# Kernel tuning notes

Hardware: AMD Instinct MI355X
Metric: run time of the kernel (lower is better)

## Reference

```python
import jax, jax.numpy as jnp
from jax import lax
import numpy as np

NUM_LABELS = 15
LABEL_TO_ID = {"O": 0, "B-PERSON": 1, "I-PERSON": 2, "B-LOCATION": 3, "I-LOCATION": 4,
               "B-ORGANIZATION": 5, "I-ORGANIZATION": 6, "B-PHONE": 7, "I-PHONE": 8,
               "B-EMAIL": 9, "I-EMAIL": 10, "B-ID_NUMBER": 11, "I-ID_NUMBER": 12,
               "B-ADDRESS": 13, "I-ADDRESS": 14}


def _pii_constraints():
    """Replicates EnhancedPIICRF._setup_transition_constraints."""
    forbidden = -10000.0
    c = np.zeros((NUM_LABELS, NUM_LABELS), dtype=np.float32)
    pii_types = ['PERSON', 'LOCATION', 'ORGANIZATION', 'PHONE', 'EMAIL', 'ID_NUMBER', 'ADDRESS']
    for t in pii_types:
        b_idx = LABEL_TO_ID[f'B-{t}']
        i_idx = LABEL_TO_ID[f'I-{t}']
        for o in pii_types:
            if o != t:
                c[LABEL_TO_ID[f'B-{o}'], i_idx] = forbidden
        if t in ['PHONE', 'EMAIL', 'ID_NUMBER']:
            c[i_idx, i_idx] = -1.0
    return jnp.asarray(c)


def setup_inputs() -> dict:
    key = jax.random.key(0)
    k1, k2, k3, k4, k5 = jax.random.split(key, 5)
    B, T, L = 512, 4096, NUM_LABELS
    emissions = jax.random.normal(k1, (B, T, L), dtype=jnp.float32)
    labels = jax.random.randint(k2, (B, T), 0, L, dtype=jnp.int64)
    mask = jnp.ones((B, T), dtype=jnp.bool_)
    # torchcrf init: uniform(-0.1, 0.1); constraints added to transitions
    transitions = jax.random.uniform(k3, (L, L), jnp.float32, -0.1, 0.1) + _pii_constraints()
    start_transitions = jax.random.uniform(k4, (L,), jnp.float32, -0.1, 0.1)
    end_transitions = jax.random.uniform(k5, (L,), jnp.float32, -0.1, 0.1)
    return {"emissions": emissions, "transitions": transitions,
            "start_transitions": start_transitions, "end_transitions": end_transitions,
            "labels": labels, "mask": mask}


def reference(emissions, transitions, start_transitions, end_transitions, labels, mask):
    """loss = -mean log-likelihood (torchcrf reduction='mean')."""
    B, T, L = emissions.shape
    maskf = mask.astype(emissions.dtype)
    labels = labels.astype(jnp.int32)

    # ---- numerator: score of the gold path (fully vectorized) ----
    em_score = jnp.take_along_axis(emissions, labels[..., None], axis=2)[..., 0]  # [B,T]
    em_score = (em_score * maskf).sum(axis=1)
    trans_score = (transitions[labels[:, :-1], labels[:, 1:]] * maskf[:, 1:]).sum(axis=1)
    seq_ends = mask.sum(axis=1).astype(jnp.int32) - 1
    last_tags = labels[jnp.arange(B), seq_ends]
    numerator = (start_transitions[labels[:, 0]] + em_score + trans_score
                 + end_transitions[last_tags])

    # ---- denominator: forward algorithm (log-sum-exp recurrence) ----
    alpha0 = start_transitions[None, :] + emissions[:, 0]  # [B,L]

    def step(alpha, xs):
        em_t, m_t = xs  # [B,L], [B]
        nxt = jax.nn.logsumexp(alpha[:, :, None] + transitions[None], axis=1) + em_t
        return jnp.where(m_t[:, None], nxt, alpha), None

    em_T = jnp.swapaxes(emissions, 0, 1)[1:]   # [T-1,B,L]
    mk_T = jnp.swapaxes(mask, 0, 1)[1:]        # [T-1,B]
    alpha, _ = lax.scan(step, alpha0, (em_T, mk_T))
    denominator = jax.nn.logsumexp(alpha + end_transitions[None, :], axis=1)

    llh = numerator - denominator
    return -jnp.mean(llh)
```

## Files before the change

### kernel.cpp

```cpp
#include <hip/hip_runtime.h>


typedef __attribute__((ext_vector_type(8))) __bf16 bf16x8;
typedef __attribute__((ext_vector_type(4))) float f32x4;
typedef __attribute__((ext_vector_type(2))) float f32x2;

#define BATCH 512
#define TLEN  4096
#define NCH   16
#define CLEN  256
#define LOG2E 1.44269504088896340736f
#define LN2   0.69314718055994530942f

__device__ __forceinline__ int pack_bf16_pair(float lo, float hi){
  return __builtin_amdgcn_perm(__float_as_uint(hi), __float_as_uint(lo), 0x07060302);
}

__global__ __launch_bounds__(256) void crf_chunk_kernel(
    const float* __restrict__ em, const float* __restrict__ trans,
    const int* __restrict__ labels,
    float* __restrict__ wsM, float* __restrict__ wsS, float* __restrict__ wsNum)
{
  const int tid   = threadIdx.x;
  const int lane  = tid & 63;
  const int col   = lane & 15;
  const int g     = lane >> 4;
  const int wid   = blockIdx.x * 4 + (tid >> 6);
  const int b     = wid >> 4;
  const int c     = wid & (NCH - 1);
  const int t0    = 1 + c * CLEN;
  const int steps = (c == NCH - 1) ? (CLEN - 1) : CLEN;
  const int colc  = (col < 15) ? col : 14;
  const long bT   = (long)b * TLEN;

  {
    const int tA = c * CLEN + lane * 4;
    const int4 lv = *reinterpret_cast<const int4*>(labels + bT + tA);
    const int lpm1 = __shfl(lv.w, lane - 1);
    const float* emA = em + (bT + tA) * 15;
    float a = 0.f;
    float a0 = emA[lv.x] + trans[lpm1 * 15 + lv.x];
    if (lane > 0) a += a0;
    a += emA[15 + lv.y] + trans[lv.x * 15 + lv.y];
    a += emA[30 + lv.z] + trans[lv.y * 15 + lv.z];
    a += emA[45 + lv.w] + trans[lv.z * 15 + lv.w];
    if (lane == 63 && c < NCH - 1){
      const int te = (c + 1) * CLEN;
      const int le = labels[bT + te];
      a += em[(bT + te) * 15 + le] + trans[lv.w * 15 + le];
    }
    #pragma unroll
    for (int off = 1; off < 64; off <<= 1) a += __shfl_xor(a, off);
    if (lane == 0) wsNum[wid] = a;
  }

  f32x2 wa01, wa23;
  {
    float wv[4];
    #pragma unroll
    for (int j = 0; j < 4; ++j){
      const int row = 4 * g + j;
      wv[j] = (row < 15 && col < 15)
            ? __builtin_amdgcn_exp2f(trans[row * 15 + col] * LOG2E) : 0.f;
    }
    wa01.x = wv[0]; wa01.y = wv[1]; wa23.x = wv[2]; wa23.y = wv[3];
  }

  union { bf16x8 v; int i[4]; } af, bfr;
  af.i[2] = 0; af.i[3] = 0;
  bfr.i[2] = 0; bfr.i[3] = 0;

  f32x4 d;
  #pragma unroll
  for (int r = 0; r < 4; ++r) d[r] = (4 * g + r == col) ? 1.f : 0.f;

  const f32x4 zero4 = {0.f, 0.f, 0.f, 0.f};
  const float* emb = em + (bT + t0) * 15 + colc;
  float S = 0.f;
  const int rounds = steps >> 3;
  const int rem    = steps & 7;
  float eb[8];

  for (int r = 0; r < rounds; ++r){
    const float* p = emb + r * 120;
    #pragma unroll
    for (int u = 0; u < 8; ++u) eb[u] = p[u * 15];
    if (r){
      float m = fmaxf(fmaxf(d[0], d[1]), fmaxf(d[2], d[3]));
      m = fmaxf(m, __shfl_xor(m, 16));
      m = fmaxf(m, __shfl_xor(m, 32));
      m = fmaxf(m, 1e-30f);
      const float sc = __builtin_amdgcn_rcpf(m);
      S += __builtin_amdgcn_logf(m);
      d[0] *= sc; d[1] *= sc; d[2] *= sc; d[3] *= sc;
    }
    #pragma unroll
    for (int u = 0; u < 8; ++u){
      const float E = __builtin_amdgcn_exp2f(eb[u] * LOG2E);
      const f32x2 e01 = wa01 * E, e23 = wa23 * E;
      af.i[0]  = pack_bf16_pair(e01.x, e01.y);
      af.i[1]  = pack_bf16_pair(e23.x, e23.y);
      bfr.i[0] = pack_bf16_pair(d[0], d[1]);
      bfr.i[1] = pack_bf16_pair(d[2], d[3]);
      d = __builtin_amdgcn_mfma_f32_16x16x32_bf16(af.v, bfr.v, zero4, 0, 0, 0);
    }
  }

  if (rem){
    const float* p = emb + rounds * 120;
    float et[7];
    #pragma unroll
    for (int u = 0; u < 7; ++u) et[u] = p[u * 15];
    float m = fmaxf(fmaxf(d[0], d[1]), fmaxf(d[2], d[3]));
    m = fmaxf(m, __shfl_xor(m, 16));
    m = fmaxf(m, __shfl_xor(m, 32));
    m = fmaxf(m, 1e-30f);
    const float sc = __builtin_amdgcn_rcpf(m);
    S += __builtin_amdgcn_logf(m);
    d[0] *= sc; d[1] *= sc; d[2] *= sc; d[3] *= sc;
    #pragma unroll
    for (int u = 0; u < 7; ++u){
      const float E = __builtin_amdgcn_exp2f(et[u] * LOG2E);
      const f32x2 e01 = wa01 * E, e23 = wa23 * E;
      af.i[0]  = pack_bf16_pair(e01.x, e01.y);
      af.i[1]  = pack_bf16_pair(e23.x, e23.y);
      bfr.i[0] = pack_bf16_pair(d[0], d[1]);
      bfr.i[1] = pack_bf16_pair(d[2], d[3]);
      d = __builtin_amdgcn_mfma_f32_16x16x32_bf16(af.v, bfr.v, zero4, 0, 0, 0);
    }
  }

  *reinterpret_cast<f32x4*>(wsM + (long)wid * 256 + lane * 4) = d;
  if (g == 0) wsS[wid * 16 + col] = S;
}

__global__ __launch_bounds__(256) void crf_combine_kernel(
    const float* __restrict__ em, const float* __restrict__ startT,
    const float* __restrict__ endT, const int* __restrict__ labels,
    const float* __restrict__ wsM, const float* __restrict__ wsS,
    const float* __restrict__ wsNum, float* __restrict__ out)
{
  const int lane = threadIdx.x & 63;
  const int b = blockIdx.x * 4 + (threadIdx.x >> 6);
  const int n = lane & 15;
  const int nc = (n < 15) ? n : 0;
  const long bT = (long)b * TLEN;

  float v = (n < 15)
          ? __builtin_amdgcn_exp2f((startT[nc] + em[bT * 15 + nc]) * LOG2E) : 0.f;
  float ST = 0.f;

  float np = wsNum[b * NCH + n];
  #pragma unroll
  for (int off = 1; off < 16; off <<= 1) np += __shfl_xor(np, off);

  const int srcl = 16 * (n >> 2) + n;

  for (int c = 0; c < NCH; ++c){
    const f32x4 m4 = *reinterpret_cast<const f32x4*>(
        wsM + ((long)(b * NCH + c)) * 256 + lane * 4);
    const float scn = wsS[(b * NCH + c) * 16 + n];
    float mu = (n < 15) ? scn : -3.0e38f;
    #pragma unroll
    for (int off = 1; off < 16; off <<= 1) mu = fmaxf(mu, __shfl_xor(mu, off));
    v = (n < 15) ? v * __builtin_amdgcn_exp2f(scn - mu) : 0.f;

    float p0 = m4[0] * v, p1 = m4[1] * v, p2 = m4[2] * v, p3 = m4[3] * v;
    #pragma unroll
    for (int off = 1; off < 16; off <<= 1){
      p0 += __shfl_xor(p0, off); p1 += __shfl_xor(p1, off);
      p2 += __shfl_xor(p2, off); p3 += __shfl_xor(p3, off);
    }
    const float ysel = (n & 2) ? ((n & 1) ? p3 : p2) : ((n & 1) ? p1 : p0);
    v = __shfl(ysel, srcl);
    ST += mu;
    float mx = v;
    #pragma unroll
    for (int off = 1; off < 16; off <<= 1) mx = fmaxf(mx, __shfl_xor(mx, off));
    v *= __builtin_amdgcn_rcpf(mx);
    ST += __builtin_amdgcn_logf(mx);
  }

  float w = (n < 15) ? v * __builtin_amdgcn_exp2f(endT[nc] * LOG2E) : 0.f;
  #pragma unroll
  for (int off = 1; off < 16; off <<= 1) w += __shfl_xor(w, off);

  if (lane == 0){
    const float den = (__builtin_amdgcn_logf(w) + ST) * LN2;
    const int l0 = labels[bT];
    const int lT = labels[bT + TLEN - 1];
    const float num = np + startT[l0] + em[bT * 15 + l0] + endT[lT];
    atomicAdd(out, (den - num) * (1.0f / BATCH));
  }
}

extern "C" void kernel_launch(void* const* d_in, const int* in_sizes, int n_in,
                              void* d_out, int out_size, void* d_ws, size_t ws_size,
                              hipStream_t stream)
{
  const float* em     = (const float*)d_in[0];
  const float* trans  = (const float*)d_in[1];
  const float* startT = (const float*)d_in[2];
  const float* endT   = (const float*)d_in[3];
  const int*   labels = (const int*)d_in[4];
  float* out = (float*)d_out;

  float* wsNum = (float*)d_ws;
  float* wsS   = (float*)((char*)d_ws + 65536);
  float* wsM   = (float*)((char*)d_ws + 65536 + 524288);

  hipMemsetAsync(d_out, 0, sizeof(float), stream);

  crf_chunk_kernel<<<BATCH * NCH / 4, 256, 0, stream>>>(em, trans, labels, wsM, wsS, wsNum);
  crf_combine_kernel<<<BATCH / 4, 256, 0, stream>>>(em, startT, endT, labels, wsM, wsS, wsNum, out);
}
```

Baseline: 284.9 us.

## Renormalize via exponent extraction folded into exp, double-buffer emission loads

Replaces the per-round max reduction with cross-lane shuffles, reciprocal, log and rescale by a power-of-two factor. The factor is taken from the exponent bits of one lane's d[0] and folded into the first step's exp2 argument, and the scale is accumulated as an integer log2. Emission loads are double-buffered so the next round's loads are issued before the current MFMA chain, and the first load is hoisted above the numerator computation. The combine kernel drops its per-chunk max reduction over scales, since each chunk now stores a single scalar. The risk is that the scale comes from a single element, so values could drift in range without true max normalization.

```diff
diff --git a/kernel.cpp b/kernel.cpp
--- a/kernel.cpp
+++ b/kernel.cpp
@@ -29,9 +29,16 @@
   const int b     = wid >> 4;
   const int c     = wid & (NCH - 1);
   const int t0    = 1 + c * CLEN;
-  const int steps = (c == NCH - 1) ? (CLEN - 1) : CLEN;
   const int colc  = (col < 15) ? col : 14;
   const long bT   = (long)b * TLEN;
+
+  const float* emb = em + (bT + t0) * 15 + colc;
+  float eb[8], ebn[8];
+
+  #define LOADE(buf, rr) { const float* _p = emb + (rr) * 120; \
+    _Pragma("unroll") for (int u = 0; u < 8; ++u) (buf)[u] = _p[u * 15]; }
+
+  LOADE(eb, 0);
 
   {
     const int tA = c * CLEN + lane * 4;
@@ -75,28 +82,21 @@
   for (int r = 0; r < 4; ++r) d[r] = (4 * g + r == col) ? 1.f : 0.f;
 
   const f32x4 zero4 = {0.f, 0.f, 0.f, 0.f};
-  const float* emb = em + (bT + t0) * 15 + colc;
-  float S = 0.f;
-  const int rounds = steps >> 3;
-  const int rem    = steps & 7;
-  float eb[8];
-
-  for (int r = 0; r < rounds; ++r){
-    const float* p = emb + r * 120;
-    #pragma unroll
-    for (int u = 0; u < 8; ++u) eb[u] = p[u * 15];
-    if (r){
-      float m = fmaxf(fmaxf(d[0], d[1]), fmaxf(d[2], d[3]));
-      m = fmaxf(m, __shfl_xor(m, 16));
-      m = fmaxf(m, __shfl_xor(m, 32));
-      m = fmaxf(m, 1e-30f);
-      const float sc = __builtin_amdgcn_rcpf(m);
-      S += __builtin_amdgcn_logf(m);
-      d[0] *= sc; d[1] *= sc; d[2] *= sc; d[3] *= sc;
+  int Ki = 0;
+
+  auto body = [&](float* ebuf, bool renorm) {
+    float addend = 0.f;
+    if (renorm){
+      const int bits = __builtin_amdgcn_readfirstlane(__float_as_int(d[0]));
+      const int K = ((bits >> 23) & 0xff) - 127;
+      Ki += K;
+      addend = (float)(-K);
     }
     #pragma unroll
     for (int u = 0; u < 8; ++u){
-      const float E = __builtin_amdgcn_exp2f(eb[u] * LOG2E);
+      const float x = (u == 0) ? __builtin_fmaf(ebuf[0], LOG2E, addend)
+                               : ebuf[u] * LOG2E;
+      const float E = __builtin_amdgcn_exp2f(x);
       const f32x2 e01 = wa01 * E, e23 = wa23 * E;
       af.i[0]  = pack_bf16_pair(e01.x, e01.y);
       af.i[1]  = pack_bf16_pair(e23.x, e23.y);
@@ -104,34 +104,53 @@
       bfr.i[1] = pack_bf16_pair(d[2], d[3]);
       d = __builtin_amdgcn_mfma_f32_16x16x32_bf16(af.v, bfr.v, zero4, 0, 0, 0);
     }
-  }
-
-  if (rem){
-    const float* p = emb + rounds * 120;
-    float et[7];
-    #pragma unroll
-    for (int u = 0; u < 7; ++u) et[u] = p[u * 15];
-    float m = fmaxf(fmaxf(d[0], d[1]), fmaxf(d[2], d[3]));
-    m = fmaxf(m, __shfl_xor(m, 16));
-    m = fmaxf(m, __shfl_xor(m, 32));
-    m = fmaxf(m, 1e-30f);
-    const float sc = __builtin_amdgcn_rcpf(m);
-    S += __builtin_amdgcn_logf(m);
-    d[0] *= sc; d[1] *= sc; d[2] *= sc; d[3] *= sc;
-    #pragma unroll
-    for (int u = 0; u < 7; ++u){
-      const float E = __builtin_amdgcn_exp2f(et[u] * LOG2E);
-      const f32x2 e01 = wa01 * E, e23 = wa23 * E;
-      af.i[0]  = pack_bf16_pair(e01.x, e01.y);
-      af.i[1]  = pack_bf16_pair(e23.x, e23.y);
-      bfr.i[0] = pack_bf16_pair(d[0], d[1]);
-      bfr.i[1] = pack_bf16_pair(d[2], d[3]);
-      d = __builtin_amdgcn_mfma_f32_16x16x32_bf16(af.v, bfr.v, zero4, 0, 0, 0);
-    }
-  }
+  };
+
+  if (c != NCH - 1){
+    #pragma unroll 1
+    for (int rr = 0; rr < 16; ++rr){
+      LOADE(ebn, 2 * rr + 1);
+      body(eb, rr != 0);
+      LOADE(eb, 2 * rr + 2);
+      body(ebn, true);
+    }
+  } else {
+    #pragma unroll 1
+    for (int rr = 0; rr < 15; ++rr){
+      LOADE(ebn, 2 * rr + 1);
+      body(eb, rr != 0);
+      LOADE(eb, 2 * rr + 2);
+      body(ebn, true);
+    }
+    float ebt[7];
+    { const float* p = emb + 31 * 120;
+      #pragma unroll
+      for (int u = 0; u < 7; ++u) ebt[u] = p[u * 15]; }
+    body(eb, true);
+    {
+      const int bits = __builtin_amdgcn_readfirstlane(__float_as_int(d[0]));
+      const int K = ((bits >> 23) & 0xff) - 127;
+      Ki += K;
+      const float addend = (float)(-K);
+      #pragma unroll
+      for (int u = 0; u < 7; ++u){
+        const float x = (u == 0) ? __builtin_fmaf(ebt[0], LOG2E, addend)
+                                 : ebt[u] * LOG2E;
+        const float E = __builtin_amdgcn_exp2f(x);
+        const f32x2 e01 = wa01 * E, e23 = wa23 * E;
+        af.i[0]  = pack_bf16_pair(e01.x, e01.y);
+        af.i[1]  = pack_bf16_pair(e23.x, e23.y);
+        bfr.i[0] = pack_bf16_pair(d[0], d[1]);
+        bfr.i[1] = pack_bf16_pair(d[2], d[3]);
+        d = __builtin_amdgcn_mfma_f32_16x16x32_bf16(af.v, bfr.v, zero4, 0, 0, 0);
+      }
+    }
+  }
+
+  #undef LOADE
 
   *reinterpret_cast<f32x4*>(wsM + (long)wid * 256 + lane * 4) = d;
-  if (g == 0) wsS[wid * 16 + col] = S;
+  if (lane == 0) wsS[wid] = (float)Ki;
 }
 
 __global__ __launch_bounds__(256) void crf_combine_kernel(
@@ -159,12 +178,6 @@
   for (int c = 0; c < NCH; ++c){
     const f32x4 m4 = *reinterpret_cast<const f32x4*>(
         wsM + ((long)(b * NCH + c)) * 256 + lane * 4);
-    const float scn = wsS[(b * NCH + c) * 16 + n];
-    float mu = (n < 15) ? scn : -3.0e38f;
-    #pragma unroll
-    for (int off = 1; off < 16; off <<= 1) mu = fmaxf(mu, __shfl_xor(mu, off));
-    v = (n < 15) ? v * __builtin_amdgcn_exp2f(scn - mu) : 0.f;
-
     float p0 = m4[0] * v, p1 = m4[1] * v, p2 = m4[2] * v, p3 = m4[3] * v;
     #pragma unroll
     for (int off = 1; off < 16; off <<= 1){
@@ -173,7 +186,7 @@
     }
     const float ysel = (n & 2) ? ((n & 1) ? p3 : p2) : ((n & 1) ? p1 : p0);
     v = __shfl(ysel, srcl);
-    ST += mu;
+    ST += wsS[b * NCH + c];
     float mx = v;
     #pragma unroll
     for (int off = 1; off < 16; off <<= 1) mx = fmaxf(mx, __shfl_xor(mx, off));
@@ -206,8 +219,8 @@
   float* out = (float*)d_out;
 
   float* wsNum = (float*)d_ws;
-  float* wsS   = (float*)((char*)d_ws + 65536);
-  float* wsM   = (float*)((char*)d_ws + 65536 + 524288);
+  float* wsS   = (float*)((char*)d_ws + 32768);
+  float* wsM   = (float*)((char*)d_ws + 65536);
 
   hipMemsetAsync(d_out, 0, sizeof(float), stream);
 
```

After: 275.6 us. 1.03x faster.
